# Performance work log

Measured on AMD Instinct MI355X. Metric: run time of the kernel, lower is better.

The kernel has to match this reference:

```python
import jax, jax.numpy as jnp
import numpy as np

EPS_LN = 1e-5
EPS_NORM = 1e-12


def _layernorm(h, g, b):
    mu = jnp.mean(h, axis=-1, keepdims=True)
    var = jnp.mean((h - mu) ** 2, axis=-1, keepdims=True)
    return (h - mu) * jax.lax.rsqrt(var + EPS_LN) * g + b


def _l2norm(h):
    n = jnp.linalg.norm(h, axis=-1, keepdims=True)
    return h / jnp.maximum(n, EPS_NORM)


def setup_inputs() -> dict:
    key = jax.random.key(0)
    ks = jax.random.split(key, 6)
    B, S, D = 8, 4096, 1024
    A, C, dc = 16, 8, 64      # n_anchors, n_comp, d_comp
    apc = A // C              # anchors per compartment = 2
    x = jax.random.normal(ks[0], (B, S, D), jnp.float32)
    anchors = jax.random.normal(ks[1], (A, D), jnp.float32)  # normalized inside forward
    ln_g = jnp.ones((D,), jnp.float32)
    ln_b = jnp.zeros((D,), jnp.float32)
    W1 = jax.random.normal(ks[2], (C, apc, 2 * dc), jnp.float32) / np.sqrt(apc)
    b1 = jnp.zeros((C, 2 * dc), jnp.float32)
    W2 = jax.random.normal(ks[3], (C, 2 * dc, dc), jnp.float32) / np.sqrt(2 * dc)
    b2 = jnp.zeros((C, dc), jnp.float32)
    cg = jnp.ones((C, dc), jnp.float32)
    cb = jnp.zeros((C, dc), jnp.float32)
    Wp = jax.random.normal(ks[4], (C * dc, D), jnp.float32) / np.sqrt(C * dc)
    bp = jnp.zeros((D,), jnp.float32)
    gate = jnp.full((D,), -3.0, jnp.float32)  # gate_init = -3.0
    return dict(x=x, anchors=anchors, ln_g=ln_g, ln_b=ln_b, W1=W1, b1=b1,
                W2=W2, b2=b2, cg=cg, cb=cb, Wp=Wp, bp=bp, gate=gate)


def reference(x, anchors, ln_g, ln_b, W1, b1, W2, b2, cg, cb, Wp, bp, gate):
    B, S, D = x.shape
    C, apc, _ = W1.shape
    dc = W2.shape[-1]
    # LayerNorm then L2-normalize each token
    h = _l2norm(_layernorm(x.reshape(B * S, D), ln_g, ln_b))  # (N, D)
    a = _l2norm(anchors)                                      # (A, D)
    tri = 1.0 - h @ a.T                                       # (N, A)
    # asgn = arange(A) % C -> comp k reads columns [k, k+C, ...]
    g = tri.reshape(-1, apc, C)                               # g[:, j, k] = tri[:, j*C + k]
    u = jnp.einsum('nak,kae->nke', g, W1) + b1                # (N, C, 2*dc)
    u = jnp.square(jnp.maximum(u, 0.0))                       # squared ReLU
    y = jnp.einsum('nke,ked->nkd', u, W2) + b2                # (N, C, dc)
    y = _layernorm(y, cg, cb)                                 # per-comp LayerNorm over dc
    y = y.reshape(-1, C * dc)                                 # concat comps in order
    update = (y @ Wp + bp).reshape(B, S, D)
    return x + jax.nn.sigmoid(gate) * update
```

## Files before the change

kernel.cpp:

```cpp
#include <hip/hip_runtime.h>
#include <hip/hip_bf16.h>

#define DIM 1024
#define NANCH 16
#define NCOMP 8
#define DC 64
#define DC2 128
#define EPS_LN 1e-5f
#define EPS_NORM 1e-12f

typedef __bf16 bf16x8 __attribute__((ext_vector_type(8)));
typedef float f32x4 __attribute__((ext_vector_type(4)));

template <int CTRL>
__device__ __forceinline__ float rr_add(float v) {
  return v + __int_as_float(__builtin_amdgcn_update_dpp(
                 0, __float_as_int(v), CTRL, 0xF, 0xF, true));
}
__device__ __forceinline__ float rowsum16(float v) {
  v = rr_add<0x121>(v);
  v = rr_add<0x122>(v);
  v = rr_add<0x124>(v);
  v = rr_add<0x128>(v);
  return v;
}
__device__ __forceinline__ float wavesum64(float v) {
  v = rowsum16(v);
  v += __shfl_xor(v, 16);
  v += __shfl_xor(v, 32);
  return v;
}

__global__ __launch_bounds__(256) void knorm_anchors(
    const float* __restrict__ anchors, float* __restrict__ An) {
  int a = blockIdx.x, t = threadIdx.x;
  int lane = t & 63, wid = t >> 6;
  __shared__ float red[4];
  float v[4]; float ss = 0.f;
#pragma unroll
  for (int i = 0; i < 4; i++) {
    v[i] = anchors[a * DIM + t + 256 * i];
    ss += v[i] * v[i];
  }
  for (int off = 32; off; off >>= 1) ss += __shfl_down(ss, off);
  if (lane == 0) red[wid] = ss;
  __syncthreads();
  float inv = 1.f / fmaxf(sqrtf(red[0] + red[1] + red[2] + red[3]), EPS_NORM);
#pragma unroll
  for (int i = 0; i < 4; i++) An[a * DIM + t + 256 * i] = v[i] * inv;
}

__global__ __launch_bounds__(256) void ktrans(
    const float* __restrict__ Wp, __hip_bfloat16* __restrict__ WpT) {
  __shared__ float tile[64][65];
  int bj = blockIdx.x, bk = blockIdx.y;
  int tx = threadIdx.x & 63, ty = threadIdx.x >> 6;
#pragma unroll
  for (int i = 0; i < 16; i++) {
    int r = ty + 4 * i;
    tile[r][tx] = Wp[(size_t)(bk * 64 + r) * DIM + bj * 64 + tx];
  }
  __syncthreads();
#pragma unroll
  for (int i = 0; i < 16; i++) {
    int r = ty + 4 * i;
    WpT[(size_t)(bj * 64 + r) * 512 + bk * 64 + tx] = __float2bfloat16(tile[tx][r]);
  }
}

__global__ __launch_bounds__(256) void kprep(
    const float* __restrict__ W2, const float* __restrict__ An,
    __hip_bfloat16* __restrict__ W2B, __hip_bfloat16* __restrict__ AnB) {
  int id = blockIdx.x * 256 + threadIdx.x;
  if (id < 65536) {
    int j = id & 7, lane = (id >> 3) & 63, ks = (id >> 9) & 3,
        nt = (id >> 11) & 3, k = id >> 13;
    int e = ks * 32 + (lane >> 4) * 8 + j;
    int n = nt * 16 + (lane & 15);
    W2B[id] = __float2bfloat16(W2[k * (DC2 * DC) + e * DC + n]);
  } else {
    int id2 = id - 65536;
    int j = id2 & 7, lane = (id2 >> 3) & 63, ks = id2 >> 9;
    int e = ks * 32 + (lane >> 4) * 8 + j;
    int a = lane & 15;
    AnB[id2] = __float2bfloat16(An[a * DIM + e]);
  }
}

#define LDA_H 1032
__global__ __launch_bounds__(256, 7) void ktoken(
    const float* __restrict__ x, const __hip_bfloat16* __restrict__ AnB,
    const float* __restrict__ ln_g, const float* __restrict__ ln_b,
    const float* __restrict__ W1, const float* __restrict__ b1,
    const __hip_bfloat16* __restrict__ W2B, const float* __restrict__ b2,
    const float* __restrict__ cg, const float* __restrict__ cb,
    __hip_bfloat16* __restrict__ yout) {
  int t = threadIdx.x;
  int lane = t & 63, w = t >> 6;
  int l15 = lane & 15, quad = lane >> 4;
  int n0 = blockIdx.x * 8;

  __shared__ __hip_bfloat16 hu[8 * LDA_H];
  __shared__ float tri_s[8 * 16];
  __shared__ float part[4 * 32 * 4];

  float gv[16], bv[16];
#pragma unroll
  for (int i = 0; i < 4; i++) {
    f32x4 g4 = *(const f32x4*)(&ln_g[i * 256 + lane * 4]);
    f32x4 b4 = *(const f32x4*)(&ln_b[i * 256 + lane * 4]);
#pragma unroll
    for (int j = 0; j < 4; j++) { gv[i * 4 + j] = g4[j]; bv[i * 4 + j] = b4[j]; }
  }
#pragma unroll
  for (int it = 0; it < 2; it++) {
    int tok = w * 2 + it;
    const float* xr = x + (size_t)(n0 + tok) * DIM;
    float xv[16], s = 0.f, s2 = 0.f;
#pragma unroll
    for (int i = 0; i < 4; i++) {
      f32x4 v4 = *(const f32x4*)(&xr[i * 256 + lane * 4]);
#pragma unroll
      for (int j = 0; j < 4; j++) {
        float v = v4[j];
        xv[i * 4 + j] = v; s += v; s2 += v * v;
      }
    }
    s = wavesum64(s);
    s2 = wavesum64(s2);
    float mu = s * (1.f / DIM);
    float rstd = rsqrtf(s2 * (1.f / DIM) - mu * mu + EPS_LN);
    float ss = 0.f;
#pragma unroll
    for (int i = 0; i < 16; i++) {
      float h = (xv[i] - mu) * rstd * gv[i] + bv[i];
      xv[i] = h; ss += h * h;
    }
    ss = wavesum64(ss);
    float inv = 1.f / fmaxf(sqrtf(ss), EPS_NORM);
#pragma unroll
    for (int i = 0; i < 4; i++) {
      union { uint2 u; __hip_bfloat16 h[4]; } pk;
#pragma unroll
      for (int j = 0; j < 4; j++) pk.h[j] = __float2bfloat16(xv[i * 4 + j] * inv);
      *(uint2*)(&hu[tok * LDA_H + i * 256 + lane * 4]) = pk.u;
    }
  }
  __syncthreads();

  {
    f32x4 tacc = {0.f, 0.f, 0.f, 0.f};
    int ar = l15 & 7;
#pragma unroll
    for (int ks = w * 8; ks < w * 8 + 8; ks++) {
      bf16x8 afr = *(const bf16x8*)(&hu[ar * LDA_H + ks * 32 + quad * 8]);
      bf16x8 bfr = *(const bf16x8*)(&AnB[ks * 512 + lane * 8]);
      tacc = __builtin_amdgcn_mfma_f32_16x16x32_bf16(afr, bfr, tacc, 0, 0, 0);
    }
    if (quad < 2) *(f32x4*)(&part[(w * 32 + (lane & 31)) * 4]) = tacc;
  }
  __syncthreads();
  if (t < 128) {
    int ln = t & 31, rg = t >> 5;
    float v = part[(0 * 32 + ln) * 4 + rg] + part[(1 * 32 + ln) * 4 + rg] +
              part[(2 * 32 + ln) * 4 + rg] + part[(3 * 32 + ln) * 4 + rg];
    int m = (ln >> 4) * 4 + rg, a = ln & 15;
    tri_s[m * 16 + a] = 1.f - v;
  }
  __syncthreads();

  {
    int k = t >> 5;
    int e0 = (t * 4) & 127;
    f32x4 w1a = *(const f32x4*)(&W1[k * 256 + e0]);
    f32x4 w1b = *(const f32x4*)(&W1[k * 256 + 128 + e0]);
    f32x4 b1v = *(const f32x4*)(&b1[k * 128 + e0]);
#pragma unroll
    for (int tok = 0; tok < 8; tok++) {
      float t0 = tri_s[tok * 16 + k], t1 = tri_s[tok * 16 + 8 + k];
      union { unsigned long long u; __hip_bfloat16 h[4]; } pk;
#pragma unroll
      for (int j = 0; j < 4; j++) {
        float uu = t0 * w1a[j] + t1 * w1b[j] + b1v[j];
        uu = fmaxf(uu, 0.f);
        pk.h[j] = __float2bfloat16(uu * uu);
      }
      *(unsigned long long*)(&hu[tok * LDA_H + t * 4]) = pk.u;
    }
  }
  __syncthreads();

#pragma unroll
  for (int kc = 0; kc < 2; kc++) {
    int k = w * 2 + kc;
    int ar = l15 & 7;
    bf16x8 afr[4];
#pragma unroll
    for (int ks = 0; ks < 4; ks++)
      afr[ks] = *(const bf16x8*)(&hu[ar * LDA_H + k * 128 + ks * 32 + quad * 8]);
    f32x4 acc[4] = {{0,0,0,0},{0,0,0,0},{0,0,0,0},{0,0,0,0}};
#pragma unroll
    for (int nt = 0; nt < 4; nt++) {
#pragma unroll
      for (int ks = 0; ks < 4; ks++) {
        bf16x8 bfr = *(const bf16x8*)(&W2B[(size_t)(((k * 4 + nt) * 4 + ks)) * 512 + lane * 8]);
        acc[nt] = __builtin_amdgcn_mfma_f32_16x16x32_bf16(afr[ks], bfr, acc[nt], 0, 0, 0);
      }
    }
    float vals[4][4], s1[4] = {0,0,0,0}, s2[4] = {0,0,0,0};
#pragma unroll
    for (int nt = 0; nt < 4; nt++) {
      float b2v = b2[k * 64 + nt * 16 + l15];
#pragma unroll
      for (int r = 0; r < 4; r++) {
        float v = acc[nt][r] + b2v;
        vals[nt][r] = v; s1[r] += v; s2[r] += v * v;
      }
    }
#pragma unroll
    for (int r = 0; r < 4; r++) {
      s1[r] = rowsum16(s1[r]);
      s2[r] = rowsum16(s2[r]);
    }
#pragma unroll
    for (int r = 0; r < 4; r++) {
      float mu = s1[r] * (1.f / DC);
      float rs = rsqrtf(s2[r] * (1.f / DC) - mu * mu + EPS_LN);
      int tokrow = quad * 4 + r;
      if (tokrow < 8) {
#pragma unroll
        for (int nt = 0; nt < 4; nt++) {
          int d = nt * 16 + l15;
          float yn = (vals[nt][r] - mu) * rs * cg[k * 64 + d] + cb[k * 64 + d];
          yout[(size_t)(n0 + tokrow) * 512 + k * 64 + d] = __float2bfloat16(yn);
        }
      }
    }
  }
}

#define LDP 72
__global__ __launch_bounds__(256) void kgemm(
    const __hip_bfloat16* __restrict__ Y, const __hip_bfloat16* __restrict__ WpT,
    const float* __restrict__ x, const float* __restrict__ bp,
    const float* __restrict__ gate, float* __restrict__ out) {
  __shared__ alignas(16) __hip_bfloat16 As[128 * LDP];
  __shared__ alignas(16) __hip_bfloat16 Bs[128 * LDP];
  int t = threadIdx.x, lane = t & 63, wid = t >> 6;
  int bm = blockIdx.x, bj = blockIdx.y;
  int wm = (wid >> 1) * 64, wj = (wid & 1) * 64;
  int l15 = lane & 15, quad = lane >> 4;

  f32x4 acc[4][4] = {};

  for (int k0 = 0; k0 < 512; k0 += 64) {
#pragma unroll
    for (int it = 0; it < 4; it++) {
      int c = it * 256 + t;
      int row = c >> 3, col = (c & 7) * 8;
      *(uint4*)(&As[row * LDP + col]) =
          *(const uint4*)(&Y[(size_t)(bm * 128 + row) * 512 + k0 + col]);
      *(uint4*)(&Bs[row * LDP + col]) =
          *(const uint4*)(&WpT[(size_t)(bj * 128 + row) * 512 + k0 + col]);
    }
    __syncthreads();
#pragma unroll
    for (int kk = 0; kk < 64; kk += 32) {
      bf16x8 af[4], bfr[4];
#pragma unroll
      for (int i = 0; i < 4; i++) {
        af[i]  = *(const bf16x8*)(&As[(wm + i * 16 + l15) * LDP + kk + quad * 8]);
        bfr[i] = *(const bf16x8*)(&Bs[(wj + i * 16 + l15) * LDP + kk + quad * 8]);
      }
#pragma unroll
      for (int i = 0; i < 4; i++)
#pragma unroll
        for (int j = 0; j < 4; j++)
          acc[i][j] = __builtin_amdgcn_mfma_f32_16x16x32_bf16(af[i], bfr[j], acc[i][j], 0, 0, 0);
    }
    __syncthreads();
  }

  float sg[4], bpv[4];
#pragma unroll
  for (int j = 0; j < 4; j++) {
    int gc = bj * 128 + wj + j * 16 + l15;
    sg[j] = 1.f / (1.f + expf(-gate[gc]));
    bpv[j] = bp[gc];
  }
#pragma unroll
  for (int i = 0; i < 4; i++) {
#pragma unroll
    for (int j = 0; j < 4; j++) {
      int gc = bj * 128 + wj + j * 16 + l15;
#pragma unroll
      for (int r = 0; r < 4; r++) {
        int gr = bm * 128 + wm + i * 16 + quad * 4 + r;
        size_t idx = (size_t)gr * DIM + gc;
        out[idx] = x[idx] + sg[j] * (acc[i][j][r] + bpv[j]);
      }
    }
  }
}

extern "C" void kernel_launch(void* const* d_in, const int* in_sizes, int n_in,
                              void* d_out, int out_size, void* d_ws, size_t ws_size,
                              hipStream_t stream) {
  const float* x       = (const float*)d_in[0];
  const float* anchors = (const float*)d_in[1];
  const float* ln_g    = (const float*)d_in[2];
  const float* ln_b    = (const float*)d_in[3];
  const float* W1      = (const float*)d_in[4];
  const float* b1      = (const float*)d_in[5];
  const float* W2      = (const float*)d_in[6];
  const float* b2      = (const float*)d_in[7];
  const float* cg      = (const float*)d_in[8];
  const float* cb      = (const float*)d_in[9];
  const float* Wp      = (const float*)d_in[10];
  const float* bp      = (const float*)d_in[11];
  const float* gate    = (const float*)d_in[12];

  int N = in_sizes[0] / DIM;

  char* w = (char*)d_ws;
  size_t off = 0;
  float* An           = (float*)(w + off);           off += 64 << 10;
  __hip_bfloat16* WpT = (__hip_bfloat16*)(w + off);  off += 1 << 20;
  __hip_bfloat16* W2B = (__hip_bfloat16*)(w + off);  off += 128 << 10;
  __hip_bfloat16* AnB = (__hip_bfloat16*)(w + off);  off += 32 << 10;
  __hip_bfloat16* Yb  = (__hip_bfloat16*)(w + off);

  knorm_anchors<<<NANCH, 256, 0, stream>>>(anchors, An);
  ktrans<<<dim3(16, 8), 256, 0, stream>>>(Wp, WpT);
  kprep<<<320, 256, 0, stream>>>(W2, An, W2B, AnB);
  ktoken<<<N / 8, 256, 0, stream>>>(x, AnB, ln_g, ln_b, W1, b1, W2B, b2, cg, cb, Yb);
  kgemm<<<dim3(N / 128, DIM / 128), 256, 0, stream>>>(Yb, WpT, x, bp, gate,
                                                      (float*)d_out);
}
```

Baseline: 355.0 us.

## Prefetch MFMA weights into registers and use swizzled direct-to-LDS loads in GEMM

In the token kernel, the anchor and W2 bf16 fragments and the x rows are now loaded into registers up front, before the barriers where they are needed, so global latency overlaps the LayerNorm and reduction phases. The occupancy hint drops from 7 to 4 to make room for the larger register footprint. In the projection GEMM, tiles go straight from global memory into LDS with global_load_lds, and an XOR swizzle replaces row padding to avoid bank conflicts. This gives up some occupancy, and correctness depends on the direct LDS load using a per-lane layout that matches the swizzle.

```diff
diff --git a/kernel.cpp b/kernel.cpp
--- a/kernel.cpp
+++ b/kernel.cpp
@@ -29,6 +29,12 @@
   v += __shfl_xor(v, 16);
   v += __shfl_xor(v, 32);
   return v;
+}
+
+__device__ __forceinline__ void gload16(const __hip_bfloat16* g, __hip_bfloat16* l) {
+  __builtin_amdgcn_global_load_lds(
+      (const __attribute__((address_space(1))) unsigned int*)g,
+      (__attribute__((address_space(3))) unsigned int*)l, 16, 0, 0);
 }
 
 __global__ __launch_bounds__(256) void knorm_anchors(
@@ -88,7 +94,7 @@
 }
 
 #define LDA_H 1032
-__global__ __launch_bounds__(256, 7) void ktoken(
+__global__ __launch_bounds__(256, 4) void ktoken(
     const float* __restrict__ x, const __hip_bfloat16* __restrict__ AnB,
     const float* __restrict__ ln_g, const float* __restrict__ ln_b,
     const float* __restrict__ W1, const float* __restrict__ b1,
@@ -104,6 +110,11 @@
   __shared__ float tri_s[8 * 16];
   __shared__ float part[4 * 32 * 4];
 
+  bf16x8 anb[8];
+#pragma unroll
+  for (int i = 0; i < 8; i++)
+    anb[i] = *(const bf16x8*)(&AnB[(w * 8 + i) * 512 + lane * 8]);
+
   float gv[16], bv[16];
 #pragma unroll
   for (int i = 0; i < 4; i++) {
@@ -112,17 +123,23 @@
 #pragma unroll
     for (int j = 0; j < 4; j++) { gv[i * 4 + j] = g4[j]; bv[i * 4 + j] = b4[j]; }
   }
+  f32x4 xv4[2][4];
+#pragma unroll
+  for (int it = 0; it < 2; it++) {
+    const float* xr = x + (size_t)(n0 + w * 2 + it) * DIM;
+#pragma unroll
+    for (int i = 0; i < 4; i++)
+      xv4[it][i] = *(const f32x4*)(&xr[i * 256 + lane * 4]);
+  }
 #pragma unroll
   for (int it = 0; it < 2; it++) {
     int tok = w * 2 + it;
-    const float* xr = x + (size_t)(n0 + tok) * DIM;
     float xv[16], s = 0.f, s2 = 0.f;
 #pragma unroll
     for (int i = 0; i < 4; i++) {
-      f32x4 v4 = *(const f32x4*)(&xr[i * 256 + lane * 4]);
 #pragma unroll
       for (int j = 0; j < 4; j++) {
-        float v = v4[j];
+        float v = xv4[it][i][j];
         xv[i * 4 + j] = v; s += v; s2 += v * v;
       }
     }
@@ -152,10 +169,10 @@
     f32x4 tacc = {0.f, 0.f, 0.f, 0.f};
     int ar = l15 & 7;
 #pragma unroll
-    for (int ks = w * 8; ks < w * 8 + 8; ks++) {
+    for (int i = 0; i < 8; i++) {
+      int ks = w * 8 + i;
       bf16x8 afr = *(const bf16x8*)(&hu[ar * LDA_H + ks * 32 + quad * 8]);
-      bf16x8 bfr = *(const bf16x8*)(&AnB[ks * 512 + lane * 8]);
-      tacc = __builtin_amdgcn_mfma_f32_16x16x32_bf16(afr, bfr, tacc, 0, 0, 0);
+      tacc = __builtin_amdgcn_mfma_f32_16x16x32_bf16(afr, anb[i], tacc, 0, 0, 0);
     }
     if (quad < 2) *(f32x4*)(&part[(w * 32 + (lane & 31)) * 4]) = tacc;
   }
@@ -167,6 +184,11 @@
     int m = (ln >> 4) * 4 + rg, a = ln & 15;
     tri_s[m * 16 + a] = 1.f - v;
   }
+
+  bf16x8 bfv[16];
+#pragma unroll
+  for (int q = 0; q < 16; q++)
+    bfv[q] = *(const bf16x8*)(&W2B[(size_t)((w * 2) * 16 + q) * 512 + lane * 8]);
   __syncthreads();
 
   {
@@ -202,10 +224,14 @@
 #pragma unroll
     for (int nt = 0; nt < 4; nt++) {
 #pragma unroll
-      for (int ks = 0; ks < 4; ks++) {
-        bf16x8 bfr = *(const bf16x8*)(&W2B[(size_t)(((k * 4 + nt) * 4 + ks)) * 512 + lane * 8]);
-        acc[nt] = __builtin_amdgcn_mfma_f32_16x16x32_bf16(afr[ks], bfr, acc[nt], 0, 0, 0);
-      }
+      for (int ks = 0; ks < 4; ks++)
+        acc[nt] = __builtin_amdgcn_mfma_f32_16x16x32_bf16(afr[ks], bfv[nt * 4 + ks],
+                                                          acc[nt], 0, 0, 0);
+    }
+    if (kc == 0) {
+#pragma unroll
+      for (int q = 0; q < 16; q++)
+        bfv[q] = *(const bf16x8*)(&W2B[(size_t)((w * 2 + 1) * 16 + q) * 512 + lane * 8]);
     }
     float vals[4][4], s1[4] = {0,0,0,0}, s2[4] = {0,0,0,0};
 #pragma unroll
@@ -239,13 +265,12 @@
   }
 }
 
-#define LDP 72
-__global__ __launch_bounds__(256) void kgemm(
+__global__ __launch_bounds__(256, 4) void kgemm(
     const __hip_bfloat16* __restrict__ Y, const __hip_bfloat16* __restrict__ WpT,
     const float* __restrict__ x, const float* __restrict__ bp,
     const float* __restrict__ gate, float* __restrict__ out) {
-  __shared__ alignas(16) __hip_bfloat16 As[128 * LDP];
-  __shared__ alignas(16) __hip_bfloat16 Bs[128 * LDP];
+  __shared__ alignas(16) __hip_bfloat16 As[128 * 64];
+  __shared__ alignas(16) __hip_bfloat16 Bs[128 * 64];
   int t = threadIdx.x, lane = t & 63, wid = t >> 6;
   int bm = blockIdx.x, bj = blockIdx.y;
   int wm = (wid >> 1) * 64, wj = (wid & 1) * 64;
@@ -253,15 +278,23 @@
 
   f32x4 acc[4][4] = {};
 
-  for (int k0 = 0; k0 < 512; k0 += 64) {
+  int srow[4], scol[4];
+#pragma unroll
+  for (int it = 0; it < 4; it++) {
+    int byteo = it * 4096 + t * 16;
+    int row = byteo >> 7, colb = byteo & 127;
+    srow[it] = row;
+    scol[it] = (colb ^ ((row & 7) << 4)) >> 1;
+  }
+
+  for (int kt = 0; kt < 8; kt++) {
+    int k0 = kt * 64;
 #pragma unroll
     for (int it = 0; it < 4; it++) {
-      int c = it * 256 + t;
-      int row = c >> 3, col = (c & 7) * 8;
-      *(uint4*)(&As[row * LDP + col]) =
-          *(const uint4*)(&Y[(size_t)(bm * 128 + row) * 512 + k0 + col]);
-      *(uint4*)(&Bs[row * LDP + col]) =
-          *(const uint4*)(&WpT[(size_t)(bj * 128 + row) * 512 + k0 + col]);
+      gload16(Y + (size_t)(bm * 128 + srow[it]) * 512 + k0 + scol[it],
+              As + (it * 4096 + t * 16) / 2);
+      gload16(WpT + (size_t)(bj * 128 + srow[it]) * 512 + k0 + scol[it],
+              Bs + (it * 4096 + t * 16) / 2);
     }
     __syncthreads();
 #pragma unroll
@@ -269,8 +302,10 @@
       bf16x8 af[4], bfr[4];
 #pragma unroll
       for (int i = 0; i < 4; i++) {
-        af[i]  = *(const bf16x8*)(&As[(wm + i * 16 + l15) * LDP + kk + quad * 8]);
-        bfr[i] = *(const bf16x8*)(&Bs[(wj + i * 16 + l15) * LDP + kk + quad * 8]);
+        int ra = wm + i * 16 + l15, rb = wj + i * 16 + l15;
+        int cb2 = (kk + quad * 8) * 2;
+        af[i]  = *(const bf16x8*)((const char*)As + ra * 128 + (cb2 ^ ((ra & 7) << 4)));
+        bfr[i] = *(const bf16x8*)((const char*)Bs + rb * 128 + (cb2 ^ ((rb & 7) << 4)));
       }
 #pragma unroll
       for (int i = 0; i < 4; i++)
```

Measured after the change: 342.1 us. 1.04x faster.
